# Kernel optimization log

Measured on AMD Instinct MI355X. Metric: run time of the kernel, lower is better.

Reference implementation:

```python
import jax, jax.numpy as jnp
import numpy as np

D_MODEL = 1024
N_LAYER = 8
VOCAB = 32000
D_INNER = 2048
D_STATE = 16
DT_RANK = 64  # ceil(d_model/16)
KCONV = 4
SEQ = 2048


def causal_depthwise_conv(u, w):
    # u: [l, d_inner], w: [d_inner, 1, K]; causal padding (K-1, 0), groups=d_inner
    x = u.T[None]  # [1, d_inner, l]
    y = jax.lax.conv_general_dilated(
        x, w, window_strides=(1,), padding=[(KCONV - 1, 0)],
        dimension_numbers=("NCH", "OIH", "NCH"), feature_group_count=u.shape[1])
    return y[0].T  # [l, d_inner]


def selective_scan(u, dt, A, B, C, Dp):
    # u,dt: [l,d_in]; A: [d_in,n]; B,C: [l,n]; D: [d_in]; bilinear discretization
    dt_A = dt[:, :, None] * A[None, :, :]          # [l, d_in, n]
    dt_B = dt[:, :, None] * B[:, None, :]          # [l, d_in, n]
    denom = 1.0 - dt_A / 2
    dA = (1.0 + dt_A / 2) / denom
    dB = dt_B / denom

    def step(h, inp):
        ui, dAi, dBi, Ci = inp
        h = dAi * h + dBi * ui[:, None]            # [d_in, n]
        return h, h @ Ci                           # y_i: [d_in]

    h0 = jnp.zeros((u.shape[1], A.shape[1]), dtype=u.dtype)
    _, y = jax.lax.scan(step, h0, (u, dA, dB, C))
    return y + u * Dp


def mamba_layer(x, Wres, Win, Wconv, WB, WC, Wdt1, Wdt2, bdt, logA, Dp, Wout):
    # RMS pre-norm (no learned scale)
    xn = x * jax.lax.rsqrt(jnp.mean(x * x, axis=-1, keepdims=True) + 1e-6)
    res = xn @ Wres.T                              # [l, d_inner]
    u = xn @ Win.T                                 # [l, d_inner]
    u = causal_depthwise_conv(u, Wconv)
    u = jax.nn.silu(u)
    A = -jnp.exp(logA)                             # [d_inner, n]
    B = u @ WB.T                                   # [l, n]
    C = u @ WC.T                                   # [l, n]
    dt = jax.nn.softplus((u @ Wdt1.T) @ Wdt2.T + bdt)
    y = selective_scan(u, dt, A, B, C, Dp)
    y = y * jax.nn.silu(res)
    return x + y @ Wout.T                          # residual


def setup_inputs() -> dict:
    key = jax.random.key(0)
    ks = jax.random.split(key, 12)
    L = N_LAYER
    token_ids = jax.random.randint(ks[0], (SEQ,), 0, VOCAB)
    embed = jax.random.normal(ks[1], (VOCAB, D_MODEL), jnp.float32) * 0.02
    Wres = jax.random.normal(ks[2], (L, D_INNER, D_MODEL), jnp.float32) * 0.02
    Win = jax.random.normal(ks[3], (L, D_INNER, D_MODEL), jnp.float32) * 0.02
    Wconv = jax.random.normal(ks[4], (L, D_INNER, 1, KCONV), jnp.float32) * 0.3
    WB = jax.random.normal(ks[5], (L, D_STATE, D_INNER), jnp.float32) * 0.02
    WC = jax.random.normal(ks[6], (L, D_STATE, D_INNER), jnp.float32) * 0.02
    Wdt1 = jax.random.normal(ks[7], (L, DT_RANK, D_INNER), jnp.float32) / np.sqrt(D_INNER)
    Wdt2 = jax.random.uniform(ks[8], (L, D_INNER, DT_RANK), jnp.float32,
                              minval=-1 / np.sqrt(DT_RANK), maxval=1 / np.sqrt(DT_RANK))
    # inverse-softplus of dt ~ U[1e-3, 1e-1] in log space
    dt0 = jnp.exp(jax.random.uniform(ks[9], (L, D_INNER)) * (np.log(0.1) - np.log(0.001)) + np.log(0.001))
    bdt = dt0 + jnp.log(-jnp.expm1(-dt0))
    logA = jnp.log(jnp.broadcast_to(jnp.arange(1, D_STATE + 1, dtype=jnp.float32),
                                    (L, D_INNER, D_STATE)))
    Dp = jnp.ones((L, D_INNER), jnp.float32)
    Wout = jax.random.normal(ks[10], (L, D_MODEL, D_INNER), jnp.float32) * 0.02
    return dict(token_ids=token_ids, embed=embed, Wres=Wres, Win=Win, Wconv=Wconv,
                WB=WB, WC=WC, Wdt1=Wdt1, Wdt2=Wdt2, bdt=bdt, logA=logA, Dp=Dp, Wout=Wout)


def reference(token_ids, embed, Wres, Win, Wconv, WB, WC, Wdt1, Wdt2, bdt, logA, Dp, Wout):
    x = embed[token_ids]  # [l, d_model]
    for i in range(Wres.shape[0]):
        x = mamba_layer(x, Wres[i], Win[i], Wconv[i], WB[i], WC[i],
                        Wdt1[i], Wdt2[i], bdt[i], logA[i], Dp[i], Wout[i])
    return x @ embed.T  # [l, vocab] logits (tied embedding)
```

## Files before the change

### kernel.cpp

```cpp
#include <hip/hip_runtime.h>

#define SEQ 2048
#define DMODEL 1024
#define DINNER 2048
#define DSTATE 16
#define DTRANK 64
#define NLAYER 8
#define VOCAB 32000
#define NCHUNK 32
#define CLEN 64
#define PROJ_NCH 16
#define PROJ_KC 128

typedef float f32x4 __attribute__((ext_vector_type(4)));
typedef short bf16x8 __attribute__((ext_vector_type(8)));

__device__ __forceinline__ ushort f2bf(float f) {
  union { float f; unsigned u; } v; v.f = f;
  unsigned r = v.u + 0x7fffu + ((v.u >> 16) & 1u);
  return (ushort)(r >> 16);
}

__device__ __forceinline__ void lds_load16(const void* g, void* l) {
  __builtin_amdgcn_global_load_lds(
      (const __attribute__((address_space(1))) void*)g,
      (__attribute__((address_space(3))) void*)l, 16, 0, 0);
}

template<bool NTS>
__global__ __launch_bounds__(256, 2) void gemm2p_bt_bf16(
    const ushort* __restrict__ A, const ushort* __restrict__ B,
    float* __restrict__ C, int N, int K)
{
  __shared__ __align__(16) ushort As[2 * 128 * 64];
  __shared__ __align__(16) ushort Bs[2 * 128 * 64];
  const int tid = threadIdx.x;
  const int lane = tid & 63;
  const int wave = tid >> 6;
  const int wr = wave >> 1, wc = wave & 1;
  const int rr = lane & 15, kq = lane >> 4;

  unsigned nwg = gridDim.x * gridDim.y;
  unsigned lb = blockIdx.y * gridDim.x + blockIdx.x;
  if ((nwg & 7u) == 0u) { unsigned cpx = nwg >> 3; lb = (lb & 7u) * cpx + (lb >> 3); }
  const int bm = (int)(lb % gridDim.x) * 128;
  const int bn = (int)(lb / gridDim.x) * 128;

  const ushort* Abase = A + (size_t)bm * K;
  const ushort* Bbase = B + (size_t)bn * K;

  auto stage = [&](int buf, int kt) {
#pragma unroll
    for (int i = 0; i < 4; ++i) {
      int f = i * 256 + tid;
      int rl = f >> 3, g = f & 7;
      int gg = g ^ (rl & 7);
      lds_load16(Abase + (size_t)rl * K + kt * 64 + gg * 8,
                 (void*)(As + buf * 8192 + rl * 64 + g * 8));
      lds_load16(Bbase + (size_t)rl * K + kt * 64 + gg * 8,
                 (void*)(Bs + buf * 8192 + rl * 64 + g * 8));
    }
  };
  auto rdA = [&](int buf, int r, int kbyte) {
    int sw = kbyte ^ ((r & 7) << 4);
    return *(const bf16x8*)(As + buf * 8192 + r * 64 + (sw >> 1));
  };
  auto rdB = [&](int buf, int r, int kbyte) {
    int sw = kbyte ^ ((r & 7) << 4);
    return *(const bf16x8*)(Bs + buf * 8192 + r * 64 + (sw >> 1));
  };

  f32x4 acc[4][4];
#pragma unroll
  for (int m = 0; m < 4; ++m)
#pragma unroll
    for (int n = 0; n < 4; ++n) acc[m][n] = (f32x4){0.f, 0.f, 0.f, 0.f};

  const int NT = K >> 6;
  stage(0, 0);

  for (int t = 0; t < NT; ++t) {
    const int cur = t & 1;
    if (t + 1 < NT) {
      stage(cur ^ 1, t + 1);
      asm volatile("s_waitcnt vmcnt(8)" ::: "memory");
    } else {
      asm volatile("s_waitcnt vmcnt(0)" ::: "memory");
    }
    __syncthreads();
#pragma unroll
    for (int ks = 0; ks < 2; ++ks) {
      const int kbyte = ks * 64 + kq * 16;
      bf16x8 af[4], bfr[4];
#pragma unroll
      for (int m = 0; m < 4; ++m)
        af[m] = rdA(cur, wr * 64 + m * 16 + rr, kbyte);
#pragma unroll
      for (int n = 0; n < 4; ++n)
        bfr[n] = rdB(cur, wc * 64 + n * 16 + rr, kbyte);
      __builtin_amdgcn_s_setprio(1);
#pragma unroll
      for (int m = 0; m < 4; ++m)
#pragma unroll
        for (int n = 0; n < 4; ++n)
          acc[m][n] = __builtin_amdgcn_mfma_f32_16x16x32_bf16(af[m], bfr[n], acc[m][n], 0, 0, 0);
      __builtin_amdgcn_s_setprio(0);
    }
    __syncthreads();
  }

  float* ep = (float*)Bs + wave * (16 * 68);
  const int cg = bn + wc * 64;
#pragma unroll
  for (int m = 0; m < 4; ++m) {
    const int r0g = bm + wr * 64 + m * 16;
#pragma unroll
    for (int n = 0; n < 4; ++n)
#pragma unroll
      for (int j = 0; j < 4; ++j)
        ep[(kq * 4 + j) * 68 + n * 16 + rr] = acc[m][n][j];
#pragma unroll
    for (int i = 0; i < 4; ++i) {
      int row = i * 4 + kq;
      f32x4 v = *(const f32x4*)&ep[row * 68 + rr * 4];
      f32x4* dst = (f32x4*)&C[(size_t)(r0g + row) * N + cg + rr * 4];
      if constexpr (NTS) __builtin_nontemporal_store(v, dst);
      else *dst = v;
    }
  }
}

__global__ __launch_bounds__(256) void gemm_btk_bf16(
    const ushort* __restrict__ A, const ushort* __restrict__ B,
    float* __restrict__ Cp, int M, int N, int K)
{
  __shared__ __align__(16) ushort As[128 * 64];
  __shared__ __align__(16) ushort Bs[128 * 64];
  const int tid = threadIdx.x;
  const int lane = tid & 63;
  const int wave = tid >> 6;
  const int wr = wave >> 1, wc = wave & 1;
  const int KC = K >> 1;
  const int k0 = blockIdx.z * KC;

  unsigned nwg = gridDim.x * gridDim.y;
  unsigned lb = blockIdx.y * gridDim.x + blockIdx.x;
  if ((nwg & 7u) == 0u) {
    unsigned cpx = nwg >> 3;
    lb = (lb & 7u) * cpx + (lb >> 3);
  }
  const int bm = (lb % gridDim.x) * 128;
  const int bn = (lb / gridDim.x) * 128;
  const int rr = lane & 15, kq = lane >> 4;

  f32x4 acc[4][4];
#pragma unroll
  for (int m = 0; m < 4; ++m)
#pragma unroll
    for (int n = 0; n < 4; ++n) acc[m][n] = (f32x4){0.f, 0.f, 0.f, 0.f};

  for (int kt = 0; kt < KC; kt += 64) {
#pragma unroll
    for (int i = 0; i < 4; ++i) {
      int fb = i * 256 + tid;
      int row = fb >> 3, cb = fb & 7;
      lds_load16(A + (size_t)(bm + row) * K + k0 + kt + cb * 8, (void*)(As + (size_t)fb * 8));
      lds_load16(B + (size_t)(bn + row) * K + k0 + kt + cb * 8, (void*)(Bs + (size_t)fb * 8));
    }
    __syncthreads();
#pragma unroll
    for (int ks = 0; ks < 2; ++ks) {
      bf16x8 af[4], bfr[4];
      const int koff = ks * 32 + kq * 8;
#pragma unroll
      for (int m = 0; m < 4; ++m)
        af[m] = *(const bf16x8*)&As[(wr * 64 + m * 16 + rr) * 64 + koff];
#pragma unroll
      for (int n = 0; n < 4; ++n)
        bfr[n] = *(const bf16x8*)&Bs[(wc * 64 + n * 16 + rr) * 64 + koff];
#pragma unroll
      for (int m = 0; m < 4; ++m)
#pragma unroll
        for (int n = 0; n < 4; ++n)
          acc[m][n] = __builtin_amdgcn_mfma_f32_16x16x32_bf16(af[m], bfr[n], acc[m][n], 0, 0, 0);
    }
    __syncthreads();
  }
  float* C = Cp + (size_t)blockIdx.z * M * N;
#pragma unroll
  for (int m = 0; m < 4; ++m) {
    const int r0 = bm + wr * 64 + m * 16 + kq * 4;
#pragma unroll
    for (int n = 0; n < 4; ++n) {
      const int cc = bn + wc * 64 + n * 16 + rr;
#pragma unroll
      for (int j = 0; j < 4; ++j)
        C[(size_t)(r0 + j) * N + cc] = acc[m][n][j];
    }
  }
}

__global__ __launch_bounds__(256) void add3_rms_kernel(
    const float* __restrict__ P0, const float* __restrict__ P1,
    float* __restrict__ x, ushort* __restrict__ dst, int donorm)
{
  size_t o = (size_t)blockIdx.x * (DMODEL / 4) + threadIdx.x;
  float4 a = ((const float4*)P0)[o];
  float4 b = ((const float4*)P1)[o];
  float4 c = ((float4*)x)[o];
  c.x += a.x + b.x; c.y += a.y + b.y; c.z += a.z + b.z; c.w += a.w + b.w;
  ((float4*)x)[o] = c;
  float sc = 1.f;
  if (donorm) {
    float s = c.x * c.x + c.y * c.y + c.z * c.z + c.w * c.w;
#pragma unroll
    for (int off = 32; off > 0; off >>= 1) s += __shfl_down(s, off);
    __shared__ float ws[4];
    if ((threadIdx.x & 63) == 0) ws[threadIdx.x >> 6] = s;
    __syncthreads();
    float tot = ws[0] + ws[1] + ws[2] + ws[3];
    sc = rsqrtf(tot * (1.0f / DMODEL) + 1e-6f);
  }
  ushort4 o4 = {f2bf(c.x * sc), f2bf(c.y * sc), f2bf(c.z * sc), f2bf(c.w * sc)};
  ((ushort4*)dst)[o] = o4;
}

__global__ __launch_bounds__(256) void gather_rms_kernel(
    const int* __restrict__ ids, const float* __restrict__ embed,
    float* __restrict__ x, ushort* __restrict__ xnb)
{
  int row = blockIdx.x;
  int id = ids[row];
  float4 v = ((const float4*)(embed + (size_t)id * DMODEL))[threadIdx.x];
  size_t o = (size_t)row * (DMODEL / 4) + threadIdx.x;
  ((float4*)x)[o] = v;
  float s = v.x * v.x + v.y * v.y + v.z * v.z + v.w * v.w;
#pragma unroll
  for (int off = 32; off > 0; off >>= 1) s += __shfl_down(s, off);
  __shared__ float ws[4];
  if ((threadIdx.x & 63) == 0) ws[threadIdx.x >> 6] = s;
  __syncthreads();
  float tot = ws[0] + ws[1] + ws[2] + ws[3];
  float sc = rsqrtf(tot * (1.0f / DMODEL) + 1e-6f);
  ushort4 o4 = {f2bf(v.x * sc), f2bf(v.y * sc), f2bf(v.z * sc), f2bf(v.w * sc)};
  ((ushort4*)xnb)[o] = o4;
}

__global__ __launch_bounds__(256) void projgemm_f32(
    const float* __restrict__ A, const float* __restrict__ W,
    float* __restrict__ Cp, int M)
{
  __shared__ float As[64][65];
  __shared__ float Ws[96][65];
  const int t = threadIdx.x;
  const int bm = blockIdx.x * 64;
  const int kc = blockIdx.y * PROJ_KC;
  const int ty = t >> 4, tx = t & 15;
  const int r0 = ty * 4, c0 = tx * 6;
  float acc[4][6] = {};
  for (int kt = 0; kt < PROJ_KC; kt += 64) {
#pragma unroll
    for (int i = 0; i < 4; ++i) {
      int e4 = i * 256 + t;
      int r = e4 >> 4, c4 = (e4 & 15) * 4;
      *(float4*)&As[r][c4] = *(const float4*)&A[(size_t)(bm + r) * DINNER + kc + kt + c4];
    }
#pragma unroll
    for (int i = 0; i < 6; ++i) {
      int e4 = i * 256 + t;
      int r = e4 >> 4, c4 = (e4 & 15) * 4;
      *(float4*)&Ws[r][c4] = *(const float4*)&W[(size_t)r * DINNER + kc + kt + c4];
    }
    __syncthreads();
#pragma unroll 4
    for (int kk = 0; kk < 64; ++kk) {
      float a0 = As[r0][kk], a1 = As[r0 + 1][kk], a2 = As[r0 + 2][kk], a3 = As[r0 + 3][kk];
      float w0 = Ws[c0][kk], w1 = Ws[c0 + 1][kk], w2 = Ws[c0 + 2][kk];
      float w3 = Ws[c0 + 3][kk], w4 = Ws[c0 + 4][kk], w5 = Ws[c0 + 5][kk];
      acc[0][0] += a0 * w0; acc[0][1] += a0 * w1; acc[0][2] += a0 * w2;
      acc[0][3] += a0 * w3; acc[0][4] += a0 * w4; acc[0][5] += a0 * w5;
      acc[1][0] += a1 * w0; acc[1][1] += a1 * w1; acc[1][2] += a1 * w2;
      acc[1][3] += a1 * w3; acc[1][4] += a1 * w4; acc[1][5] += a1 * w5;
      acc[2][0] += a2 * w0; acc[2][1] += a2 * w1; acc[2][2] += a2 * w2;
      acc[2][3] += a2 * w3; acc[2][4] += a2 * w4; acc[2][5] += a2 * w5;
      acc[3][0] += a3 * w0; acc[3][1] += a3 * w1; acc[3][2] += a3 * w2;
      acc[3][3] += a3 * w3; acc[3][4] += a3 * w4; acc[3][5] += a3 * w5;
    }
    __syncthreads();
  }
  float* cp = Cp + (size_t)blockIdx.y * M * 96;
#pragma unroll
  for (int i = 0; i < 4; ++i)
#pragma unroll
    for (int j = 0; j < 6; ++j)
      cp[(size_t)(bm + r0 + i) * 96 + c0 + j] = acc[i][j];
}

__global__ __launch_bounds__(256) void proj_reduce(
    const float* __restrict__ Cp, float* __restrict__ bcdt, int M)
{
  int idx = blockIdx.x * 256 + threadIdx.x;
  float s = 0.f;
#pragma unroll
  for (int c = 0; c < PROJ_NCH; ++c) s += Cp[(size_t)c * M * 96 + idx];
  bcdt[idx] = s;
}

__global__ __launch_bounds__(256) void smallgemm_f32(
    const float* __restrict__ A, int lda,
    const float* __restrict__ W, int ldw,
    float* __restrict__ C, int ldc,
    const float* __restrict__ bias,
    int M, int N, int K, int act)
{
  __shared__ float As[64][65];
  __shared__ float Ws[64][65];
  const int t = threadIdx.x;
  const int bm = blockIdx.x * 64, bn = blockIdx.y * 64;
  const int r0 = (t >> 4) * 4;
  const int c0 = (t & 15) * 4;
  float acc[4][4] = {};

  for (int kt = 0; kt < K; kt += 64) {
#pragma unroll
    for (int i = 0; i < 16; ++i) {
      int idx = i * 256 + t;
      int r = idx >> 6, c = idx & 63;
      As[r][c] = A[(size_t)(bm + r) * lda + kt + c];
      int wrow = bn + r;
      Ws[r][c] = (wrow < N) ? W[(size_t)wrow * ldw + kt + c] : 0.f;
    }
    __syncthreads();
#pragma unroll 8
    for (int kk = 0; kk < 64; ++kk) {
      float a0 = As[r0][kk], a1 = As[r0 + 1][kk], a2 = As[r0 + 2][kk], a3 = As[r0 + 3][kk];
      float w0 = Ws[c0][kk], w1 = Ws[c0 + 1][kk], w2 = Ws[c0 + 2][kk], w3 = Ws[c0 + 3][kk];
      acc[0][0] += a0 * w0; acc[0][1] += a0 * w1; acc[0][2] += a0 * w2; acc[0][3] += a0 * w3;
      acc[1][0] += a1 * w0; acc[1][1] += a1 * w1; acc[1][2] += a1 * w2; acc[1][3] += a1 * w3;
      acc[2][0] += a2 * w0; acc[2][1] += a2 * w1; acc[2][2] += a2 * w2; acc[2][3] += a2 * w3;
      acc[3][0] += a3 * w0; acc[3][1] += a3 * w1; acc[3][2] += a3 * w2; acc[3][3] += a3 * w3;
    }
    __syncthreads();
  }
#pragma unroll
  for (int i = 0; i < 4; ++i)
#pragma unroll
    for (int j = 0; j < 4; ++j) {
      int cc = bn + c0 + j;
      if (cc < N) {
        float v = acc[i][j];
        if (bias) v += bias[cc];
        if (act == 1) v = (v > 20.f) ? v : log1pf(expf(v));
        C[(size_t)(bm + r0 + i) * ldc + cc] = v;
      }
    }
}

__global__ __launch_bounds__(256) void conv_silu_kernel(
    const float* __restrict__ u0, int ld, const float* __restrict__ Wconv,
    float* __restrict__ u)
{
  int idx = blockIdx.x * 256 + threadIdx.x;
  int d4 = idx & (DINNER / 4 - 1);
  int l = idx >> 9;
  int d0 = d4 * 4;
  float wt[4][4];
#pragma unroll
  for (int j = 0; j < 4; ++j) {
    float4 tv = *(const float4*)&Wconv[(d0 + j) * 4];
    wt[j][0] = tv.x; wt[j][1] = tv.y; wt[j][2] = tv.z; wt[j][3] = tv.w;
  }
  float a[4] = {0.f, 0.f, 0.f, 0.f};
#pragma unroll
  for (int k = 0; k < 4; ++k) {
    int ls = l - 3 + k;
    if (ls >= 0) {
      float4 uv = *(const float4*)&u0[(size_t)ls * ld + d0];
      a[0] += uv.x * wt[0][k];
      a[1] += uv.y * wt[1][k];
      a[2] += uv.z * wt[2][k];
      a[3] += uv.w * wt[3][k];
    }
  }
  float4 r;
  r.x = a[0] / (1.f + expf(-a[0]));
  r.y = a[1] / (1.f + expf(-a[1]));
  r.z = a[2] / (1.f + expf(-a[2]));
  r.w = a[3] / (1.f + expf(-a[3]));
  *(float4*)&u[(size_t)l * DINNER + d0] = r;
}

__global__ __launch_bounds__(256) void scan_pass1(
    const float* __restrict__ dt, const float* __restrict__ u,
    const float* __restrict__ bcdt, const float* __restrict__ logA,
    float* __restrict__ P, float* __restrict__ S)
{
  const int tid = threadIdx.x;
  const int n = tid & 15, dl = tid >> 4;
  const int dbase = blockIdx.x * 16;
  const int c = blockIdx.y;
  const int t0 = c * CLEN;
  const int d = dbase + dl;
  const float Aval = -expf(logA[d * DSTATE + n]);
  __shared__ float sdt[CLEN][16], su[CLEN][16], sB[CLEN][16];
  {
    int tt = tid >> 2, j0 = (tid & 3) * 4;
    *(float4*)&sdt[tt][j0] = *(const float4*)&dt[(size_t)(t0 + tt) * DINNER + dbase + j0];
    *(float4*)&su[tt][j0]  = *(const float4*)&u[(size_t)(t0 + tt) * DINNER + dbase + j0];
    *(float4*)&sB[tt][j0]  = *(const float4*)&bcdt[(size_t)(t0 + tt) * 96 + j0];
  }
  __syncthreads();
  float h = 0.f, pr = 1.f;
#pragma unroll 8
  for (int i = 0; i < CLEN; ++i) {
    float dtv = sdt[i][dl], uv = su[i][dl], Bv = sB[i][n];
    float dtA = dtv * Aval;
    float rinv = __builtin_amdgcn_rcpf(1.f - 0.5f * dtA);
    float dA = (1.f + 0.5f * dtA) * rinv;
    float dBu = dtv * Bv * rinv * uv;
    h = dA * h + dBu;
    pr *= dA;
  }
  size_t idx = (size_t)c * (DINNER * DSTATE) + (size_t)d * DSTATE + n;
  P[idx] = pr;
  S[idx] = h;
}

__global__ __launch_bounds__(256) void scan_pass2(
    const float* __restrict__ dt, const float* __restrict__ u,
    const float* __restrict__ bcdt, const float* __restrict__ logA,
    const float* __restrict__ Dp, const float* __restrict__ P,
    const float* __restrict__ S, const float* __restrict__ resu0,
    ushort* __restrict__ y2b)
{
  const int tid = threadIdx.x;
  const int n = tid & 15, dl = tid >> 4;
  const int dbase = blockIdx.x * 16;
  const int c = blockIdx.y;
  const int t0 = c * CLEN;
  const int d = dbase + dl;
  const float Aval = -expf(logA[d * DSTATE + n]);
  const float Dpv = Dp[d];
  __shared__ float sdt[CLEN][16], su[CLEN][16], sB[CLEN][16], sC[CLEN][16], sres[CLEN][16];
  {
    int tt = tid >> 2, j0 = (tid & 3) * 4;
    *(float4*)&sdt[tt][j0]  = *(const float4*)&dt[(size_t)(t0 + tt) * DINNER + dbase + j0];
    *(float4*)&su[tt][j0]   = *(const float4*)&u[(size_t)(t0 + tt) * DINNER + dbase + j0];
    *(float4*)&sB[tt][j0]   = *(const float4*)&bcdt[(size_t)(t0 + tt) * 96 + j0];
    *(float4*)&sC[tt][j0]   = *(const float4*)&bcdt[(size_t)(t0 + tt) * 96 + 16 + j0];
    *(float4*)&sres[tt][j0] = *(const float4*)&resu0[(size_t)(t0 + tt) * (2 * DINNER) + dbase + j0];
  }
  float h = 0.f;
  {
    const size_t base = (size_t)d * DSTATE + n;
#pragma unroll 4
    for (int cc = 0; cc < c; ++cc) {
      size_t o = (size_t)cc * (DINNER * DSTATE) + base;
      h = P[o] * h + S[o];
    }
  }
  __syncthreads();
#pragma unroll 4
  for (int i = 0; i < CLEN; ++i) {
    float dtv = sdt[i][dl], uv = su[i][dl];
    float dtA = dtv * Aval;
    float rinv = __builtin_amdgcn_rcpf(1.f - 0.5f * dtA);
    float dA = (1.f + 0.5f * dtA) * rinv;
    float dBu = dtv * sB[i][n] * rinv * uv;
    h = dA * h + dBu;
    float p = h * sC[i][n];
    p += __shfl_xor(p, 1);
    p += __shfl_xor(p, 2);
    p += __shfl_xor(p, 4);
    p += __shfl_xor(p, 8);
    if (n == 0) {
      float rv = sres[i][dl];
      float yv = (p + uv * Dpv) * (rv / (1.f + expf(-rv)));
      y2b[(size_t)(t0 + i) * DINNER + d] = f2bf(yv);
    }
  }
}

__global__ __launch_bounds__(256) void cast_bf16_kernel(
    const float* __restrict__ in, ushort* __restrict__ out, size_t n4)
{
  size_t i = (size_t)blockIdx.x * 256 + threadIdx.x;
  if (i >= n4) return;
  float4 v = ((const float4*)in)[i];
  ushort4 o = {f2bf(v.x), f2bf(v.y), f2bf(v.z), f2bf(v.w)};
  ((ushort4*)out)[i] = o;
}

__global__ __launch_bounds__(256) void cast_cat2_kernel(
    const float* __restrict__ Wres, const float* __restrict__ Win, ushort* __restrict__ out)
{
  size_t i4 = (size_t)blockIdx.x * 256 + threadIdx.x;
  size_t e0 = i4 * 4;
  int k = (int)(e0 & (DMODEL - 1));
  int r = (int)((e0 >> 10) & (2 * DINNER - 1));
  int l = (int)(e0 >> 22);
  const float* src = (r < DINNER)
      ? &Wres[(((size_t)l * DINNER + r) << 10) + k]
      : &Win[(((size_t)l * DINNER + (r - DINNER)) << 10) + k];
  float4 v = *(const float4*)src;
  ushort4 o = {f2bf(v.x), f2bf(v.y), f2bf(v.z), f2bf(v.w)};
  ((ushort4*)out)[i4] = o;
}

__global__ __launch_bounds__(256) void concat_wbcdt_kernel(
    const float* __restrict__ WB, const float* __restrict__ WC,
    const float* __restrict__ Wdt1, float* __restrict__ out)
{
  size_t idx = (size_t)blockIdx.x * 256 + threadIdx.x;
  int k = idx & (DINNER - 1);
  size_t rl = idx >> 11;
  int row = (int)(rl % 96);
  int l = (int)(rl / 96);
  float v;
  if (row < 16)       v = WB[((size_t)l * DSTATE + row) * DINNER + k];
  else if (row < 32)  v = WC[((size_t)l * DSTATE + (row - 16)) * DINNER + k];
  else                v = Wdt1[((size_t)l * DTRANK + (row - 32)) * DINNER + k];
  out[idx] = v;
}

extern "C" void kernel_launch(void* const* d_in, const int* in_sizes, int n_in,
                              void* d_out, int out_size, void* d_ws, size_t ws_size,
                              hipStream_t stream) {
  (void)in_sizes; (void)n_in; (void)out_size;
  const int* token_ids = (const int*)d_in[0];
  const float* embed = (const float*)d_in[1];
  const float* Wres = (const float*)d_in[2];
  const float* Win = (const float*)d_in[3];
  const float* Wconv = (const float*)d_in[4];
  const float* WB = (const float*)d_in[5];
  const float* WC = (const float*)d_in[6];
  const float* Wdt1 = (const float*)d_in[7];
  const float* Wdt2 = (const float*)d_in[8];
  const float* bdt = (const float*)d_in[9];
  const float* logA = (const float*)d_in[10];
  const float* Dp = (const float*)d_in[11];
  const float* Wout = (const float*)d_in[12];
  float* out = (float*)d_out;

  char* w = (char*)d_ws;
  auto alloc = [&](size_t bytes) {
    char* p = w;
    w += (bytes + 255) & ~(size_t)255;
    return p;
  };
  ushort* eb    = (ushort*)alloc((size_t)VOCAB * DMODEL * 2);
  ushort* wcatb = (ushort*)alloc((size_t)NLAYER * 2 * DINNER * DMODEL * 2);
  ushort* woutb = (ushort*)alloc((size_t)NLAYER * DMODEL * DINNER * 2);
  float* wbcdt  = (float*)alloc((size_t)NLAYER * 96 * DINNER * 4);
  float* x      = (float*)alloc((size_t)SEQ * DMODEL * 4);
  ushort* xnb   = (ushort*)alloc((size_t)SEQ * DMODEL * 2);
  float* resu0  = (float*)alloc((size_t)SEQ * 2 * DINNER * 4);
  float* u      = (float*)alloc((size_t)SEQ * DINNER * 4);
  float* bcdt   = (float*)alloc((size_t)SEQ * 96 * 4);
  float* dt     = (float*)alloc((size_t)SEQ * DINNER * 4);
  float* Cp     = (float*)alloc((size_t)PROJ_NCH * SEQ * 96 * 4);
  float* Cp2    = (float*)alloc((size_t)2 * SEQ * DMODEL * 4);
  float* Pbuf   = (float*)alloc((size_t)NCHUNK * DINNER * DSTATE * 4);
  float* Sbuf   = (float*)alloc((size_t)NCHUNK * DINNER * DSTATE * 4);
  ushort* y2b   = (ushort*)alloc((size_t)SEQ * DINNER * 2);
  ushort* xb    = (ushort*)alloc((size_t)SEQ * DMODEL * 2);
  if ((size_t)(w - (char*)d_ws) > ws_size) return;

  cast_bf16_kernel<<<VOCAB * DMODEL / 4 / 256, 256, 0, stream>>>(embed, eb, (size_t)VOCAB * DMODEL / 4);
  cast_cat2_kernel<<<NLAYER * 2 * DINNER * DMODEL / 4 / 256, 256, 0, stream>>>(Wres, Win, wcatb);
  cast_bf16_kernel<<<NLAYER * DMODEL * DINNER / 4 / 256, 256, 0, stream>>>(Wout, woutb, (size_t)NLAYER * DMODEL * DINNER / 4);
  concat_wbcdt_kernel<<<NLAYER * 96 * DINNER / 256, 256, 0, stream>>>(WB, WC, Wdt1, wbcdt);
  gather_rms_kernel<<<SEQ, 256, 0, stream>>>(token_ids, embed, x, xnb);

  for (int i = 0; i < NLAYER; ++i) {
    const ushort* wcati = wcatb + (size_t)i * 2 * DINNER * DMODEL;
    const ushort* wouti = woutb + (size_t)i * DMODEL * DINNER;
    const float* wconvi = Wconv + (size_t)i * DINNER * 4;
    const float* wbcdti = wbcdt + (size_t)i * 96 * DINNER;
    const float* wdt2i = Wdt2 + (size_t)i * DINNER * DTRANK;
    const float* bdti = bdt + (size_t)i * DINNER;
    const float* logAi = logA + (size_t)i * DINNER * DSTATE;
    const float* Dpi = Dp + (size_t)i * DINNER;

    gemm2p_bt_bf16<false><<<dim3(SEQ / 128, 2 * DINNER / 128), 256, 0, stream>>>(
        xnb, wcati, resu0, 2 * DINNER, DMODEL);
    conv_silu_kernel<<<SEQ * DINNER / 4 / 256, 256, 0, stream>>>(resu0 + DINNER, 2 * DINNER, wconvi, u);
    projgemm_f32<<<dim3(SEQ / 64, PROJ_NCH), 256, 0, stream>>>(u, wbcdti, Cp, SEQ);
    proj_reduce<<<SEQ * 96 / 256, 256, 0, stream>>>(Cp, bcdt, SEQ);
    smallgemm_f32<<<dim3(SEQ / 64, DINNER / 64), 256, 0, stream>>>(
        bcdt + 32, 96, wdt2i, DTRANK, dt, DINNER, bdti, SEQ, DINNER, DTRANK, 1);
    dim3 gs(DINNER / 16, NCHUNK);
    scan_pass1<<<gs, 256, 0, stream>>>(dt, u, bcdt, logAi, Pbuf, Sbuf);
    scan_pass2<<<gs, 256, 0, stream>>>(dt, u, bcdt, logAi, Dpi, Pbuf, Sbuf, resu0, y2b);
    gemm_btk_bf16<<<dim3(SEQ / 128, DMODEL / 128, 2), 256, 0, stream>>>(
        y2b, wouti, Cp2, SEQ, DMODEL, DINNER);
    add3_rms_kernel<<<SEQ, 256, 0, stream>>>(
        Cp2, Cp2 + (size_t)SEQ * DMODEL, x,
        (i < NLAYER - 1) ? xnb : xb, (i < NLAYER - 1) ? 1 : 0);
  }
  gemm2p_bt_bf16<true><<<dim3(SEQ / 128, VOCAB / 128), 256, 0, stream>>>(
      xb, eb, out, VOCAB, DMODEL);
}
```

Baseline: 2.268 ms.

## Use 256x256-tile 8-wave GEMM for final vocab logits projection

Adds a new bf16 MFMA GEMM kernel with 512 threads and 256x256 output tiles, with staged global-to-LDS loads interleaved between MFMA groups and s_setprio around the math. It replaces the 128x128 kernel for the final tied-embedding logits GEMM (2048x32000x1024). Larger tiles raise arithmetic intensity and cut redundant A/B loads, at the cost of more LDS and register pressure per workgroup and fewer workgroups (8x125).

```diff
diff --git a/kernel.cpp b/kernel.cpp
--- a/kernel.cpp
+++ b/kernel.cpp
@@ -25,6 +25,135 @@
   __builtin_amdgcn_global_load_lds(
       (const __attribute__((address_space(1))) void*)g,
       (__attribute__((address_space(3))) void*)l, 16, 0, 0);
+}
+
+template<int BM, bool NTS>
+__global__ __launch_bounds__(512, 2) void gemm8p_bt_bf16(
+    const ushort* __restrict__ A, const ushort* __restrict__ B,
+    float* __restrict__ C, int N, int K)
+{
+  constexpr int MFR = BM / 32;
+  constexpr int MPP = MFR / 4;
+  constexpr int ALOADS = BM / 128;
+  __shared__ __align__(16) ushort As[2 * BM * 64];
+  __shared__ __align__(16) ushort Bs[2 * 256 * 64];
+  const int tid = threadIdx.x;
+  const int lane = tid & 63;
+  const int wid = tid >> 6;
+  const int wr = wid >> 2, wc = wid & 3;
+  const int rr = lane & 15, kq = lane >> 4;
+
+  unsigned nwg = gridDim.x * gridDim.y;
+  unsigned lb = blockIdx.y * gridDim.x + blockIdx.x;
+  if ((nwg & 7u) == 0u) { unsigned cpx = nwg >> 3; lb = (lb & 7u) * cpx + (lb >> 3); }
+  const int bm = (int)(lb % gridDim.x) * BM;
+  const int bn = (int)(lb / gridDim.x) * 256;
+
+  const ushort* Abase = A + (size_t)bm * K;
+  const ushort* Bbase = B + (size_t)bn * K;
+
+  auto stageA = [&](int buf, int h, int kt) {
+    constexpr int HR = BM / 2;
+#pragma unroll
+    for (int L = 0; L < ALOADS; ++L) {
+      int f = L * 512 + tid;
+      int rl = f >> 3, g = f & 7;
+      int gg = g ^ (rl & 7);
+      lds_load16(Abase + (size_t)(h * HR + rl) * K + kt * 64 + gg * 8,
+                 (void*)(As + buf * (BM * 64) + (h * HR + rl) * 64 + g * 8));
+    }
+  };
+  auto stageB = [&](int buf, int h, int kt) {
+#pragma unroll
+    for (int L = 0; L < 2; ++L) {
+      int f = L * 512 + tid;
+      int rl = f >> 3, g = f & 7;
+      int gg = g ^ (rl & 7);
+      lds_load16(Bbase + (size_t)(h * 128 + rl) * K + kt * 64 + gg * 8,
+                 (void*)(Bs + buf * (256 * 64) + (h * 128 + rl) * 64 + g * 8));
+    }
+  };
+  auto rdA = [&](int buf, int r, int kbyte) {
+    int sw = kbyte ^ ((r & 7) << 4);
+    return *(const bf16x8*)(As + buf * (BM * 64) + r * 64 + (sw >> 1));
+  };
+  auto rdB = [&](int buf, int r, int kbyte) {
+    int sw = kbyte ^ ((r & 7) << 4);
+    return *(const bf16x8*)(Bs + buf * (256 * 64) + r * 64 + (sw >> 1));
+  };
+
+  f32x4 acc[MFR][4];
+#pragma unroll
+  for (int m = 0; m < MFR; ++m)
+#pragma unroll
+    for (int n = 0; n < 4; ++n) acc[m][n] = (f32x4){0.f, 0.f, 0.f, 0.f};
+
+  const int NT = K >> 6;
+  stageA(0, 0, 0); stageA(0, 1, 0); stageB(0, 0, 0); stageB(0, 1, 0);
+
+  for (int t = 0; t < NT; ++t) {
+    const int cur = t & 1;
+    const bool more = (t + 1 < NT);
+    if (more) stageA(cur ^ 1, 0, t + 1);
+    if (more) {
+      if constexpr (BM == 256) asm volatile("s_waitcnt vmcnt(2)" ::: "memory");
+      else                     asm volatile("s_waitcnt vmcnt(1)" ::: "memory");
+    } else {
+      asm volatile("s_waitcnt vmcnt(0)" ::: "memory");
+    }
+    __syncthreads();
+
+    bf16x8 bfr[4][2];
+#pragma unroll
+    for (int n = 0; n < 4; ++n)
+#pragma unroll
+      for (int kk = 0; kk < 2; ++kk)
+        bfr[n][kk] = rdB(cur, wc * 64 + n * 16 + rr, kk * 64 + kq * 16);
+
+#pragma unroll
+    for (int mq = 0; mq < 4; ++mq) {
+      if (mq == 1 && more) stageA(cur ^ 1, 1, t + 1);
+      if (mq == 2 && more) stageB(cur ^ 1, 0, t + 1);
+      if (mq == 3 && more) stageB(cur ^ 1, 1, t + 1);
+      bf16x8 af[MPP][2];
+#pragma unroll
+      for (int mf = 0; mf < MPP; ++mf)
+#pragma unroll
+        for (int kk = 0; kk < 2; ++kk)
+          af[mf][kk] = rdA(cur, wr * (BM / 2) + (mq * MPP + mf) * 16 + rr, kk * 64 + kq * 16);
+      __builtin_amdgcn_s_setprio(1);
+#pragma unroll
+      for (int kk = 0; kk < 2; ++kk)
+#pragma unroll
+        for (int mf = 0; mf < MPP; ++mf)
+#pragma unroll
+          for (int n = 0; n < 4; ++n)
+            acc[mq * MPP + mf][n] = __builtin_amdgcn_mfma_f32_16x16x32_bf16(
+                af[mf][kk], bfr[n][kk], acc[mq * MPP + mf][n], 0, 0, 0);
+      __builtin_amdgcn_s_setprio(0);
+    }
+    __syncthreads();
+  }
+
+  float* ep = (float*)Bs + wid * (16 * 68);
+  const int cg = bn + wc * 64;
+#pragma unroll
+  for (int m = 0; m < MFR; ++m) {
+    const int r0g = bm + wr * (BM / 2) + m * 16;
+#pragma unroll
+    for (int n = 0; n < 4; ++n)
+#pragma unroll
+      for (int j = 0; j < 4; ++j)
+        ep[(kq * 4 + j) * 68 + n * 16 + rr] = acc[m][n][j];
+#pragma unroll
+    for (int i = 0; i < 4; ++i) {
+      int row = i * 4 + kq;
+      f32x4 v = *(const f32x4*)&ep[row * 68 + rr * 4];
+      f32x4* dst = (f32x4*)&C[(size_t)(r0g + row) * N + cg + rr * 4];
+      if constexpr (NTS) __builtin_nontemporal_store(v, dst);
+      else *dst = v;
+    }
+  }
 }
 
 template<bool NTS>
@@ -598,6 +727,6 @@
         Cp2, Cp2 + (size_t)SEQ * DMODEL, x,
         (i < NLAYER - 1) ? xnb : xb, (i < NLAYER - 1) ? 1 : 0);
   }
-  gemm2p_bt_bf16<true><<<dim3(SEQ / 128, VOCAB / 128), 256, 0, stream>>>(
+  gemm8p_bt_bf16<256, true><<<dim3(SEQ / 256, VOCAB / 256), 512, 0, stream>>>(
       xb, eb, out, VOCAB, DMODEL);
 }
```

Measured after the change: 2.228 ms. Within noise of the previous version (-1.8%).
